# Kernel tuning notes

Hardware: AMD Instinct MI355X
Metric: run time of the kernel (lower is better)

The kernel has to match this reference:

```python
import jax, jax.numpy as jnp
import numpy as np

COULOMB_CONSTANT = -1.0
EV = 1.602e-19
MAX_ELEMENT = 100
N_ATOMS = 4096
HIDDEN = 16
EMB_ROWS = MAX_ELEMENT * (MAX_ELEMENT + 1) // 2  # 5050


def setup_inputs() -> dict:
    key = jax.random.key(0)
    ks = jax.random.split(key, 8)
    coordinates = jax.random.normal(ks[0], (N_ATOMS, 3), dtype=jnp.float32) * 5.0
    atom_ix = jax.random.randint(ks[1], (N_ATOMS,), 0, MAX_ELEMENT)
    charges = jax.random.normal(ks[2], (N_ATOMS,), dtype=jnp.float32)
    # embedding table [EMB_ROWS, 1]
    emb = jax.random.normal(ks[3], (EMB_ROWS, 1), dtype=jnp.float32)
    # FeedforwardNetwork sizes [2] + [16] + [3]: Linear(2,16), ReLU, Linear(16,3)
    W1 = jax.random.normal(ks[4], (2, HIDDEN), dtype=jnp.float32) / np.sqrt(2.0)
    b1 = jnp.zeros((HIDDEN,), dtype=jnp.float32)
    W2 = jax.random.normal(ks[5], (HIDDEN, 3), dtype=jnp.float32) / np.sqrt(HIDDEN)
    b2 = jnp.zeros((3,), dtype=jnp.float32)
    bias = jax.random.normal(ks[6], (1,), dtype=jnp.float32)
    return {"coordinates": coordinates, "atom_ix": atom_ix, "charges": charges,
            "emb": emb, "W1": W1, "b1": b1, "W2": W2, "b2": b2, "bias": bias}


def reference(coordinates, atom_ix, charges, emb, W1, b1, W2, b2, bias):
    # pairwise distances [N, N]
    diff = coordinates[None, :, :] - coordinates[:, None, :]
    sq = jnp.sum(diff * diff, axis=-1)
    pos = sq > 0
    d_safe = jnp.sqrt(jnp.where(pos, sq, 1.0))
    # torch: nan_to_num(1/d, 0.0) maps diagonal inf -> huge -> clamped to 10
    reciprocal_d = jnp.where(pos, jnp.minimum(1.0 / d_safe, 10.0), 10.0)
    # pairwise embedding gather: index i*(i+1)//2 + j
    pairwise_atom_ix = atom_ix[:, None] * (atom_ix[:, None] + 1) // 2 + atom_ix[None, :]
    pairwise_atom_emb = emb[pairwise_atom_ix, 0]  # [N, N]
    pairwise_charges = charges[:, None] * charges[None, :]  # [N, N]
    model_inputs = jnp.stack([pairwise_atom_emb, pairwise_charges], axis=-1)  # [N, N, 2]
    # tiny MLP: 2 -> 16 -> 3
    h = jax.nn.relu(jnp.einsum('nmi,ih->nmh', model_inputs, W1) + b1)
    atom_weights = jnp.einsum('nmh,ho->nmo', h, W2) + b2  # [N, N, 3]
    c_weights = atom_weights[..., 0]
    lj_sigma = atom_weights[..., 1]
    lj_r = atom_weights[..., 2]
    c_energy = COULOMB_CONSTANT * jnp.sum(c_weights * reciprocal_d)
    sr = lj_sigma * reciprocal_d
    sr6 = sr ** 6
    lj_energy = EV * jnp.sum(lj_r * (sr6 * sr6 - sr6))
    return c_energy + lj_energy + bias
```

## Files before the change

kernel.cpp:

```cpp
#include <hip/hip_runtime.h>
#include <hip/hip_bf16.h>
#include <stdint.h>

#define THREADS 256
#define ROWS_PER_BLOCK 8
#define JSPLIT 4
#define MAXEL 100
#define EMB_ROWS 5050

typedef _Float16 half2v __attribute__((ext_vector_type(2)));
typedef __fp16   fp16x2 __attribute__((ext_vector_type(2)));
typedef unsigned int uint4v __attribute__((ext_vector_type(4)));

__device__ __forceinline__ half2v pk(float a, float b) {
    fp16x2 r = __builtin_amdgcn_cvt_pkrtz(a, b);
    return __builtin_bit_cast(half2v, r);
}
__device__ __forceinline__ half2v pkfma(half2v a, half2v b, half2v c) {
    return __builtin_elementwise_fma(a, b, c);
}

__global__ __launch_bounds__(THREADS, 4) void energy_main_kernel(
    const float* __restrict__ coords,
    const int*   __restrict__ atom_ix,
    const float* __restrict__ charges,
    const float* __restrict__ emb,
    const float* __restrict__ W1,
    const float* __restrict__ b1,
    const float* __restrict__ W2,
    const float* __restrict__ b2,
    float* __restrict__ partials,
    int n_atoms)
{
    half2v A2[8], B2[8], C2[8], U0_2[8], U1_2[8], U2_2[8];
#pragma unroll
    for (int p = 0; p < 8; ++p) {
        A2[p]   = pk(W1[2 * p],      W1[2 * p + 1]);
        B2[p]   = pk(W1[16 + 2 * p], W1[16 + 2 * p + 1]);
        C2[p]   = pk(b1[2 * p],      b1[2 * p + 1]);
        U0_2[p] = pk(W2[3 * (2 * p) + 0], W2[3 * (2 * p + 1) + 0]);
        U1_2[p] = pk(W2[3 * (2 * p) + 1], W2[3 * (2 * p + 1) + 1]);
        U2_2[p] = pk(W2[3 * (2 * p) + 2], W2[3 * (2 * p + 1) + 2]);
    }
    const float bo0 = b2[0], bo1 = b2[1], bo2 = b2[2];

    const int rb   = blockIdx.x / JSPLIT;
    const int js   = blockIdx.x % JSPLIT;
    const int row0 = rb * ROWS_PER_BLOCK;
    const int jlen = n_atoms / JSPLIT;
    const int j0   = js * jlen;

    __shared__ uint32_t s_tab[ROWS_PER_BLOCK * MAXEL * 8];
    for (int idx = threadIdx.x; idx < ROWS_PER_BLOCK * MAXEL; idx += THREADS) {
        const int r = idx / MAXEL;
        const int a = idx - r * MAXEL;
        const int ai = atom_ix[row0 + r];
        const float e = emb[((ai * (ai + 1)) >> 1) + a];
        const half2v e2 = pk(e, e);
        uint4v w0, w1;
#pragma unroll
        for (int p = 0; p < 4; ++p)
            w0[p] = __builtin_bit_cast(uint32_t, pkfma(e2, A2[p], C2[p]));
#pragma unroll
        for (int p = 0; p < 4; ++p)
            w1[p] = __builtin_bit_cast(uint32_t, pkfma(e2, A2[p + 4], C2[p + 4]));
        *(uint4v*)&s_tab[idx * 8 + 0] = w0;
        *(uint4v*)&s_tab[idx * 8 + 4] = w1;
    }

    float xr[ROWS_PER_BLOCK], yr[ROWS_PER_BLOCK], zr[ROWS_PER_BLOCK], qr[ROWS_PER_BLOCK];
#pragma unroll
    for (int r = 0; r < ROWS_PER_BLOCK; ++r) {
        const int i = row0 + r;
        xr[r] = coords[3 * i + 0];
        yr[r] = coords[3 * i + 1];
        zr[r] = coords[3 * i + 2];
        qr[r] = charges[i];
    }
    __syncthreads();

    float cacc = 0.0f, ljacc = 0.0f;
    const half2v zero2 = (half2v)(_Float16)0.0f;

#pragma unroll 1
    for (int j = j0 + threadIdx.x; j < j0 + jlen; j += THREADS) {
        const float xj = coords[3 * j + 0];
        const float yj = coords[3 * j + 1];
        const float zj = coords[3 * j + 2];
        const float qj = charges[j];
        const int   tb = atom_ix[j] * 8;

#pragma unroll
        for (int r = 0; r < ROWS_PER_BLOCK; ++r) {
            const float dx = xj - xr[r];
            const float dy = yj - yr[r];
            const float dz = zj - zr[r];
            const float sq = fmaf(dx, dx, fmaf(dy, dy, dz * dz));
            const float rd = fminf(rsqrtf(sq), 10.0f);

            const float c = qr[r] * qj;
            const half2v c2 = pk(c, c);

            const uint4v w0 = *(const uint4v*)&s_tab[r * MAXEL * 8 + tb + 0];
            const uint4v w1 = *(const uint4v*)&s_tab[r * MAXEL * 8 + tb + 4];

            float o0 = bo0, o1 = bo1, o2 = bo2;
#pragma unroll
            for (int p = 0; p < 8; ++p) {
                const uint32_t aw = (p < 4) ? w0[p] : w1[p - 4];
                half2v t = pkfma(c2, B2[p], __builtin_bit_cast(half2v, aw));
                t = __builtin_elementwise_max(t, zero2);
                o0 = __builtin_amdgcn_fdot2(t, U0_2[p], o0, false);
                o1 = __builtin_amdgcn_fdot2(t, U1_2[p], o1, false);
                o2 = __builtin_amdgcn_fdot2(t, U2_2[p], o2, false);
            }

            cacc = fmaf(o0, rd, cacc);
            const float sr  = o1 * rd;
            const float sr2 = sr * sr;
            const float sr6 = sr2 * sr2 * sr2;
            ljacc = fmaf(o2, fmaf(sr6, sr6, -sr6), ljacc);
        }
    }

#pragma unroll
    for (int off = 32; off > 0; off >>= 1) {
        cacc  += __shfl_down(cacc, off, 64);
        ljacc += __shfl_down(ljacc, off, 64);
    }
    __shared__ float s_c[THREADS / 64], s_l[THREADS / 64];
    const int wave = threadIdx.x >> 6;
    const int lane = threadIdx.x & 63;
    if (lane == 0) { s_c[wave] = cacc; s_l[wave] = ljacc; }
    __syncthreads();
    if (threadIdx.x == 0) {
        float ct = 0.0f, lt = 0.0f;
#pragma unroll
        for (int w = 0; w < THREADS / 64; ++w) { ct += s_c[w]; lt += s_l[w]; }
        partials[2 * blockIdx.x + 0] = ct;
        partials[2 * blockIdx.x + 1] = lt;
    }
}

__global__ __launch_bounds__(THREADS, 1) void energy_reduce_kernel(
    const float* __restrict__ partials, int nblocks,
    const float* __restrict__ bias, float* __restrict__ out)
{
    float ct = 0.0f, lt = 0.0f;
    for (int b = threadIdx.x; b < nblocks; b += THREADS) {
        ct += partials[2 * b + 0];
        lt += partials[2 * b + 1];
    }
#pragma unroll
    for (int off = 32; off > 0; off >>= 1) {
        ct += __shfl_down(ct, off, 64);
        lt += __shfl_down(lt, off, 64);
    }
    __shared__ float s_c[THREADS / 64], s_l[THREADS / 64];
    const int wave = threadIdx.x >> 6;
    const int lane = threadIdx.x & 63;
    if (lane == 0) { s_c[wave] = ct; s_l[wave] = lt; }
    __syncthreads();
    if (threadIdx.x == 0) {
        float c = 0.0f, l = 0.0f;
#pragma unroll
        for (int w = 0; w < THREADS / 64; ++w) { c += s_c[w]; l += s_l[w]; }
        out[0] = -c + 1.602e-19f * l + bias[0];
    }
}

extern "C" void kernel_launch(void* const* d_in, const int* in_sizes, int n_in,
                              void* d_out, int out_size, void* d_ws, size_t ws_size,
                              hipStream_t stream)
{
    const float* coords  = (const float*)d_in[0];
    const int*   atom_ix = (const int*)d_in[1];
    const float* charges = (const float*)d_in[2];
    const float* emb     = (const float*)d_in[3];
    const float* W1      = (const float*)d_in[4];
    const float* b1      = (const float*)d_in[5];
    const float* W2      = (const float*)d_in[6];
    const float* b2      = (const float*)d_in[7];
    const float* bias    = (const float*)d_in[8];

    float* out      = (float*)d_out;
    float* partials = (float*)d_ws;

    const int n       = in_sizes[1];
    const int nblocks = (n / ROWS_PER_BLOCK) * JSPLIT;

    energy_main_kernel<<<nblocks, THREADS, 0, stream>>>(
        coords, atom_ix, charges, emb, W1, b1, W2, b2, partials, n);
    energy_reduce_kernel<<<1, THREADS, 0, stream>>>(partials, nblocks, bias, out);
}
```

Measured before the change: 43.81 us.

## Replace per-row hidden-layer table with full fp16 embedding table in LDS

Instead of precomputing an 8-row by 100-element table of first-layer pre-activations (32 bytes per entry), the kernel stages the whole 5050-entry embedding table in LDS as packed fp16 pairs. The inner loop now does a 4-byte LDS load per pair plus an extra packed FMA per hidden pair, trading more ALU work for less LDS traffic and smaller shared memory. It also computes the charge product in fp16, uses the raw rsq builtin, and pins the bias vector in VGPRs with an empty asm. Staging 5050 entries per block adds setup cost, and the fp16 charge product slightly lowers precision.

```diff
diff --git a/kernel.cpp b/kernel.cpp
--- a/kernel.cpp
+++ b/kernel.cpp
@@ -5,12 +5,10 @@
 #define THREADS 256
 #define ROWS_PER_BLOCK 8
 #define JSPLIT 4
-#define MAXEL 100
 #define EMB_ROWS 5050
 
 typedef _Float16 half2v __attribute__((ext_vector_type(2)));
 typedef __fp16   fp16x2 __attribute__((ext_vector_type(2)));
-typedef unsigned int uint4v __attribute__((ext_vector_type(4)));
 
 __device__ __forceinline__ half2v pk(float a, float b) {
     fp16x2 r = __builtin_amdgcn_cvt_pkrtz(a, b);
@@ -32,12 +30,20 @@
     float* __restrict__ partials,
     int n_atoms)
 {
-    half2v A2[8], B2[8], C2[8], U0_2[8], U1_2[8], U2_2[8];
+    __shared__ uint32_t s_emb2[EMB_ROWS];
+    for (int t = threadIdx.x; t < EMB_ROWS; t += THREADS) {
+        const float e = emb[t];
+        s_emb2[t] = __builtin_bit_cast(uint32_t, pk(e, e));
+    }
+
+    half2v A2[8], B2[8], U0_2[8], U1_2[8], U2_2[8];
+    uint32_t C2v[8];
 #pragma unroll
     for (int p = 0; p < 8; ++p) {
         A2[p]   = pk(W1[2 * p],      W1[2 * p + 1]);
         B2[p]   = pk(W1[16 + 2 * p], W1[16 + 2 * p + 1]);
-        C2[p]   = pk(b1[2 * p],      b1[2 * p + 1]);
+        C2v[p]  = __builtin_bit_cast(uint32_t, pk(b1[2 * p], b1[2 * p + 1]));
+        asm("" : "+v"(C2v[p]));
         U0_2[p] = pk(W2[3 * (2 * p) + 0], W2[3 * (2 * p + 1) + 0]);
         U1_2[p] = pk(W2[3 * (2 * p) + 1], W2[3 * (2 * p + 1) + 1]);
         U2_2[p] = pk(W2[3 * (2 * p) + 2], W2[3 * (2 * p + 1) + 2]);
@@ -50,32 +56,19 @@
     const int jlen = n_atoms / JSPLIT;
     const int j0   = js * jlen;
 
-    __shared__ uint32_t s_tab[ROWS_PER_BLOCK * MAXEL * 8];
-    for (int idx = threadIdx.x; idx < ROWS_PER_BLOCK * MAXEL; idx += THREADS) {
-        const int r = idx / MAXEL;
-        const int a = idx - r * MAXEL;
-        const int ai = atom_ix[row0 + r];
-        const float e = emb[((ai * (ai + 1)) >> 1) + a];
-        const half2v e2 = pk(e, e);
-        uint4v w0, w1;
-#pragma unroll
-        for (int p = 0; p < 4; ++p)
-            w0[p] = __builtin_bit_cast(uint32_t, pkfma(e2, A2[p], C2[p]));
-#pragma unroll
-        for (int p = 0; p < 4; ++p)
-            w1[p] = __builtin_bit_cast(uint32_t, pkfma(e2, A2[p + 4], C2[p + 4]));
-        *(uint4v*)&s_tab[idx * 8 + 0] = w0;
-        *(uint4v*)&s_tab[idx * 8 + 4] = w1;
-    }
-
-    float xr[ROWS_PER_BLOCK], yr[ROWS_PER_BLOCK], zr[ROWS_PER_BLOCK], qr[ROWS_PER_BLOCK];
+    float  xr[ROWS_PER_BLOCK], yr[ROWS_PER_BLOCK], zr[ROWS_PER_BLOCK];
+    half2v qr2[ROWS_PER_BLOCK];
+    int    br[ROWS_PER_BLOCK];
 #pragma unroll
     for (int r = 0; r < ROWS_PER_BLOCK; ++r) {
         const int i = row0 + r;
         xr[r] = coords[3 * i + 0];
         yr[r] = coords[3 * i + 1];
         zr[r] = coords[3 * i + 2];
-        qr[r] = charges[i];
+        const float q = charges[i];
+        qr2[r] = pk(q, q);
+        const int a = atom_ix[i];
+        br[r] = (a * (a + 1)) >> 1;
     }
     __syncthreads();
 
@@ -88,7 +81,8 @@
         const float yj = coords[3 * j + 1];
         const float zj = coords[3 * j + 2];
         const float qj = charges[j];
-        const int   tb = atom_ix[j] * 8;
+        const half2v qj2 = pk(qj, qj);
+        const int   aj = atom_ix[j];
 
 #pragma unroll
         for (int r = 0; r < ROWS_PER_BLOCK; ++r) {
@@ -96,19 +90,16 @@
             const float dy = yj - yr[r];
             const float dz = zj - zr[r];
             const float sq = fmaf(dx, dx, fmaf(dy, dy, dz * dz));
-            const float rd = fminf(rsqrtf(sq), 10.0f);
+            const float rd = fminf(__builtin_amdgcn_rsqf(sq), 10.0f);
 
-            const float c = qr[r] * qj;
-            const half2v c2 = pk(c, c);
-
-            const uint4v w0 = *(const uint4v*)&s_tab[r * MAXEL * 8 + tb + 0];
-            const uint4v w1 = *(const uint4v*)&s_tab[r * MAXEL * 8 + tb + 4];
+            const half2v e2 = __builtin_bit_cast(half2v, s_emb2[br[r] + aj]);
+            const half2v c2 = qr2[r] * qj2;
 
             float o0 = bo0, o1 = bo1, o2 = bo2;
 #pragma unroll
             for (int p = 0; p < 8; ++p) {
-                const uint32_t aw = (p < 4) ? w0[p] : w1[p - 4];
-                half2v t = pkfma(c2, B2[p], __builtin_bit_cast(half2v, aw));
+                half2v t = pkfma(c2, B2[p], __builtin_bit_cast(half2v, C2v[p]));
+                t = pkfma(e2, A2[p], t);
                 t = __builtin_elementwise_max(t, zero2);
                 o0 = __builtin_amdgcn_fdot2(t, U0_2[p], o0, false);
                 o1 = __builtin_amdgcn_fdot2(t, U1_2[p], o1, false);
```

New measurement: 43.98 us. No clear change (+0.4%).
